# Optimization experiments

Hardware: AMD Instinct MI355X
Metric: run time of the kernel (lower is better)

Reference implementation:

```python
import jax, jax.numpy as jnp
import numpy as np

BN_EPS = 1e-5
N_IN, N_OUT = 200000, 400000
K, M, C_IN, C_OUT = 27, 100000, 64, 64


def setup_inputs() -> dict:
    key = jax.random.key(0)
    ks = jax.random.split(key, 4)
    x = jax.random.normal(ks[0], (N_IN, C_IN), dtype=jnp.float32)
    W = jax.random.normal(ks[1], (K, C_IN, C_OUT), dtype=jnp.float32) * 0.05
    gamma = jnp.ones((C_OUT,), dtype=jnp.float32)
    beta = jnp.zeros((C_OUT,), dtype=jnp.float32)
    in_idx = jax.random.randint(ks[2], (K, M), 0, N_IN, dtype=jnp.int32)
    out_idx = jax.random.randint(ks[3], (K, M), 0, N_OUT, dtype=jnp.int32)
    return {"x": x, "W": W, "gamma": gamma, "beta": beta,
            "in_idx": in_idx, "out_idx": out_idx, "n_out": N_OUT}


def reference(x, W, gamma, beta, in_idx, out_idx, n_out):
    # Sparse transposed conv via gather-GEMM-scatter over K kernel offsets.
    feats = x[in_idx]                               # [K, M, C_in] gather
    contrib = jnp.einsum('kmi,kio->kmo', feats, W)  # per-offset GEMM
    out = jnp.zeros((n_out, contrib.shape[-1]), dtype=x.dtype)
    out = out.at[out_idx.reshape(-1)].add(contrib.reshape(-1, contrib.shape[-1]))
    # BatchNorm (training-mode batch stats over all output points), gamma=1, beta=0 at init.
    mean = jnp.mean(out, axis=0)
    var = jnp.var(out, axis=0)
    y = (out - mean) * jax.lax.rsqrt(var + BN_EPS) * gamma + beta
    return jax.nn.relu(y)
```

## Files before the change

kernel.cpp:

```cpp
#include <hip/hip_runtime.h>
#include <hip/hip_bf16.h>

#define K_OFF 27
#define M_PTS 100000
#define C_CH 64
#define N_OUT_PTS 400000
#define BN_EPS 1e-5f

#define TILE_PTS 16
#define NT (M_PTS / TILE_PTS)
#define BLKX 32
#define WSTRIDE (BLKX * 4)

typedef __attribute__((ext_vector_type(8))) short short8;
typedef __attribute__((ext_vector_type(4))) float f32x4;

__device__ inline void pk_atomic_add_bf16(__hip_bfloat16* p, int bits) {
#if __has_builtin(__builtin_amdgcn_global_atomic_fadd_v2bf16)
    typedef short s2v __attribute__((ext_vector_type(2)));
    typedef __attribute__((address_space(1))) s2v* gp;
    s2v v;
    __builtin_memcpy(&v, &bits, 4);
    __builtin_amdgcn_global_atomic_fadd_v2bf16((gp)(unsigned long long)p, v);
#else
    asm volatile("global_atomic_pk_add_bf16 %0, %1, off"
                 :: "v"((unsigned long long)p), "v"(bits) : "memory");
#endif
}

__device__ inline short bf16c(float f) {
    return __builtin_bit_cast(short, __float2bfloat16(f));
}

__device__ __attribute__((always_inline)) inline void tile_compute(
    const float4* cur, const int* dstv, const short8 bfrag[2][4],
    __hip_bfloat16* __restrict__ out_ws, int c)
{
    short8 af0, af1;
    #pragma unroll
    for (int j = 0; j < 4; ++j) {
        af0[j]     = bf16c(cur[0][j]);
        af0[j + 4] = bf16c(cur[1][j]);
        af1[j]     = bf16c(cur[2][j]);
        af1[j + 4] = bf16c(cur[3][j]);
    }
    f32x4 acc[4];
    #pragma unroll
    for (int tt = 0; tt < 4; ++tt) {
        f32x4 z = {0.f, 0.f, 0.f, 0.f};
        z       = __builtin_amdgcn_mfma_f32_16x16x32_bf16(af0, bfrag[0][tt], z, 0, 0, 0);
        acc[tt] = __builtin_amdgcn_mfma_f32_16x16x32_bf16(af1, bfrag[1][tt], z, 0, 0, 0);
    }
    #pragma unroll
    for (int e = 0; e < 4; ++e) {
        __hip_bfloat16* rp = out_ws + (size_t)dstv[e] * C_CH + 4 * c;
        union { __hip_bfloat162 h; int i; } p0, p1;
        p0.h = __hip_bfloat162(__float2bfloat16(acc[0][e]), __float2bfloat16(acc[1][e]));
        p1.h = __hip_bfloat162(__float2bfloat16(acc[2][e]), __float2bfloat16(acc[3][e]));
        pk_atomic_add_bf16(rp, p0.i);
        pk_atomic_add_bf16(rp + 2, p1.i);
    }
}

__global__ __launch_bounds__(256, 4) void scatter_gemm(
    const float* __restrict__ x, const float* __restrict__ W,
    const int* __restrict__ in_idx, const int* __restrict__ out_idx,
    __hip_bfloat16* __restrict__ out_ws)
{
    const int k = blockIdx.y;
    const int lane = threadIdx.x & 63;
    const int wave = threadIdx.x >> 6;
    const int g = lane >> 4;
    const int c = lane & 15;

    const float* __restrict__ Wk = W + (size_t)k * C_CH * C_CH;
    short8 bfrag[2][4];
    #pragma unroll
    for (int s = 0; s < 2; ++s) {
        #pragma unroll
        for (int tt = 0; tt < 4; ++tt) {
            short8 v;
            #pragma unroll
            for (int j = 0; j < 8; ++j)
                v[j] = bf16c(Wk[(size_t)(32 * s + 8 * g + j) * C_CH + 4 * c + tt]);
            bfrag[s][tt] = v;
        }
    }

    const int kbase = k * M_PTS;
    const int t0 = blockIdx.x * 4 + wave;

    int src_c = in_idx[kbase + t0 * TILE_PTS + c];
    int dstv[4];
    #pragma unroll
    for (int e = 0; e < 4; ++e)
        dstv[e] = out_idx[kbase + t0 * TILE_PTS + 4 * g + e];
    float4 cur[4];
    {
        const float4* xr = (const float4*)x + (size_t)src_c * 16;
        cur[0] = xr[2 * g];     cur[1] = xr[2 * g + 1];
        cur[2] = xr[8 + 2 * g]; cur[3] = xr[8 + 2 * g + 1];
    }
    int src_n = (t0 + WSTRIDE < NT) ? in_idx[kbase + (t0 + WSTRIDE) * TILE_PTS + c] : 0;

    int t = t0;
    for (; t + WSTRIDE < NT; t += WSTRIDE) {
        const int tn = t + WSTRIDE;
        float4 nxt[4]; int dstn[4];
        {
            const float4* xr = (const float4*)x + (size_t)src_n * 16;
            nxt[0] = xr[2 * g];     nxt[1] = xr[2 * g + 1];
            nxt[2] = xr[8 + 2 * g]; nxt[3] = xr[8 + 2 * g + 1];
            #pragma unroll
            for (int e = 0; e < 4; ++e)
                dstn[e] = out_idx[kbase + tn * TILE_PTS + 4 * g + e];
        }
        const int t2 = tn + WSTRIDE;
        const int src_2 = (t2 < NT) ? in_idx[kbase + t2 * TILE_PTS + c] : 0;

        tile_compute(cur, dstv, bfrag, out_ws, c);

        #pragma unroll
        for (int j = 0; j < 4; ++j) cur[j] = nxt[j];
        #pragma unroll
        for (int e = 0; e < 4; ++e) dstv[e] = dstn[e];
        src_c = src_n;
        src_n = src_2;
    }
    tile_compute(cur, dstv, bfrag, out_ws, c);
}

__global__ __launch_bounds__(256) void bn_stats(
    const __hip_bfloat16* __restrict__ ws, float* __restrict__ stats)
{
    const uint4* in = (const uint4*)ws;
    const size_t n = (size_t)N_OUT_PTS * C_CH / 8;
    const size_t stride = (size_t)gridDim.x * blockDim.x;
    float s[8], s2[8];
    #pragma unroll
    for (int j = 0; j < 8; ++j) { s[j] = 0.f; s2[j] = 0.f; }
    for (size_t i = (size_t)blockIdx.x * blockDim.x + threadIdx.x; i < n; i += stride) {
        uint4 q = in[i];
        unsigned wds[4] = {q.x, q.y, q.z, q.w};
        #pragma unroll
        for (int j = 0; j < 4; ++j) {
            __hip_bfloat162 h = *(__hip_bfloat162*)&wds[j];
            float f0 = __low2float(h), f1 = __high2float(h);
            s[2 * j] += f0;  s2[2 * j] += f0 * f0;
            s[2 * j + 1] += f1; s2[2 * j + 1] += f1 * f1;
        }
    }
    __shared__ float sh[2][256][8];
    #pragma unroll
    for (int j = 0; j < 8; ++j) { sh[0][threadIdx.x][j] = s[j]; sh[1][threadIdx.x][j] = s2[j]; }
    __syncthreads();
    if (threadIdx.x < C_CH) {
        const int c = threadIdx.x;
        float ts = 0.f, t2 = 0.f;
        #pragma unroll
        for (int q = 0; q < 32; ++q) {
            ts += sh[0][8 * q + (c >> 3)][c & 7];
            t2 += sh[1][8 * q + (c >> 3)][c & 7];
        }
        unsafeAtomicAdd(&stats[c], ts);
        unsafeAtomicAdd(&stats[C_CH + c], t2);
    }
}

__global__ __launch_bounds__(256) void bn_apply(
    const __hip_bfloat16* __restrict__ ws, const float* __restrict__ stats,
    const float* __restrict__ gamma, const float* __restrict__ beta,
    float* __restrict__ out)
{
    const float inv_n = 1.0f / (float)N_OUT_PTS;
    const int c0 = 8 * (threadIdx.x & 7);
    float sc[8], bs[8];
    #pragma unroll
    for (int j = 0; j < 8; ++j) {
        int c = c0 + j;
        float mean = stats[c] * inv_n;
        float var = stats[C_CH + c] * inv_n - mean * mean;
        float s = gamma[c] * rsqrtf(var + BN_EPS);
        sc[j] = s;
        bs[j] = beta[c] - mean * s;
    }
    const uint4* in = (const uint4*)ws;
    float4* o4 = (float4*)out;
    const size_t n = (size_t)N_OUT_PTS * C_CH / 8;
    const size_t stride = (size_t)gridDim.x * blockDim.x;
    for (size_t i = (size_t)blockIdx.x * blockDim.x + threadIdx.x; i < n; i += stride) {
        uint4 q = in[i];
        unsigned wds[4] = {q.x, q.y, q.z, q.w};
        float f[8];
        #pragma unroll
        for (int j = 0; j < 4; ++j) {
            __hip_bfloat162 h = *(__hip_bfloat162*)&wds[j];
            f[2 * j] = __low2float(h);
            f[2 * j + 1] = __high2float(h);
        }
        float4 r0, r1;
        r0.x = fmaxf(fmaf(f[0], sc[0], bs[0]), 0.f);
        r0.y = fmaxf(fmaf(f[1], sc[1], bs[1]), 0.f);
        r0.z = fmaxf(fmaf(f[2], sc[2], bs[2]), 0.f);
        r0.w = fmaxf(fmaf(f[3], sc[3], bs[3]), 0.f);
        r1.x = fmaxf(fmaf(f[4], sc[4], bs[4]), 0.f);
        r1.y = fmaxf(fmaf(f[5], sc[5], bs[5]), 0.f);
        r1.z = fmaxf(fmaf(f[6], sc[6], bs[6]), 0.f);
        r1.w = fmaxf(fmaf(f[7], sc[7], bs[7]), 0.f);
        o4[2 * i] = r0;
        o4[2 * i + 1] = r1;
    }
}

extern "C" void kernel_launch(void* const* d_in, const int* in_sizes, int n_in,
                              void* d_out, int out_size, void* d_ws, size_t ws_size,
                              hipStream_t stream) {
    const float* x      = (const float*)d_in[0];
    const float* W      = (const float*)d_in[1];
    const float* gamma  = (const float*)d_in[2];
    const float* beta   = (const float*)d_in[3];
    const int*   in_idx = (const int*)d_in[4];
    const int*   out_idx= (const int*)d_in[5];
    float* out = (float*)d_out;

    __hip_bfloat16* out_ws = (__hip_bfloat16*)d_ws;
    const size_t acc_elems = (size_t)N_OUT_PTS * C_CH;
    float* stats = (float*)((char*)d_ws + acc_elems * sizeof(__hip_bfloat16));

    const size_t clear_bytes = acc_elems * sizeof(__hip_bfloat16) + 2 * C_CH * sizeof(float);
    (void)hipMemsetAsync(d_ws, 0, clear_bytes, stream);

    dim3 g1(BLKX, K_OFF);
    scatter_gemm<<<g1, 256, 0, stream>>>(x, W, in_idx, out_idx, out_ws);

    bn_stats<<<2048, 256, 0, stream>>>(out_ws, stats);

    bn_apply<<<2048, 256, 0, stream>>>(out_ws, stats, gamma, beta, out);
}
```

Measured before the change: 766.2 us.

## Replace atomic scatter with binned gather: dense contrib GEMM plus per-output reduction

```diff
diff --git a/kernel.cpp b/kernel.cpp
--- a/kernel.cpp
+++ b/kernel.cpp
@@ -3,17 +3,26 @@
 
 #define K_OFF 27
 #define M_PTS 100000
+#define KM (K_OFF * M_PTS)
 #define C_CH 64
 #define N_OUT_PTS 400000
 #define BN_EPS 1e-5f
 
 #define TILE_PTS 16
 #define NT (M_PTS / TILE_PTS)
-#define BLKX 32
+#define BLKX 64
 #define WSTRIDE (BLKX * 4)
+#define CAP 40
 
 typedef __attribute__((ext_vector_type(8))) short short8;
 typedef __attribute__((ext_vector_type(4))) float f32x4;
+
+__device__ inline short bf16c(float f) {
+    return __builtin_bit_cast(short, __float2bfloat16(f));
+}
+__device__ inline float b2f(unsigned short u) {
+    return __builtin_bit_cast(float, (unsigned)u << 16);
+}
 
 __device__ inline void pk_atomic_add_bf16(__hip_bfloat16* p, int bits) {
 #if __has_builtin(__builtin_amdgcn_global_atomic_fadd_v2bf16)
@@ -28,13 +37,8 @@
 #endif
 }
 
-__device__ inline short bf16c(float f) {
-    return __builtin_bit_cast(short, __float2bfloat16(f));
-}
-
-__device__ __attribute__((always_inline)) inline void tile_compute(
-    const float4* cur, const int* dstv, const short8 bfrag[2][4],
-    __hip_bfloat16* __restrict__ out_ws, int c)
+__device__ __attribute__((always_inline)) inline void tile_mfma(
+    const float4* cur, const short8 bfrag[2][4], f32x4 acc[4])
 {
     short8 af0, af1;
     #pragma unroll
@@ -44,37 +48,17 @@
         af1[j]     = bf16c(cur[2][j]);
         af1[j + 4] = bf16c(cur[3][j]);
     }
-    f32x4 acc[4];
     #pragma unroll
     for (int tt = 0; tt < 4; ++tt) {
         f32x4 z = {0.f, 0.f, 0.f, 0.f};
         z       = __builtin_amdgcn_mfma_f32_16x16x32_bf16(af0, bfrag[0][tt], z, 0, 0, 0);
         acc[tt] = __builtin_amdgcn_mfma_f32_16x16x32_bf16(af1, bfrag[1][tt], z, 0, 0, 0);
     }
-    #pragma unroll
-    for (int e = 0; e < 4; ++e) {
-        __hip_bfloat16* rp = out_ws + (size_t)dstv[e] * C_CH + 4 * c;
-        union { __hip_bfloat162 h; int i; } p0, p1;
-        p0.h = __hip_bfloat162(__float2bfloat16(acc[0][e]), __float2bfloat16(acc[1][e]));
-        p1.h = __hip_bfloat162(__float2bfloat16(acc[2][e]), __float2bfloat16(acc[3][e]));
-        pk_atomic_add_bf16(rp, p0.i);
-        pk_atomic_add_bf16(rp + 2, p1.i);
-    }
-}
-
-__global__ __launch_bounds__(256, 4) void scatter_gemm(
-    const float* __restrict__ x, const float* __restrict__ W,
-    const int* __restrict__ in_idx, const int* __restrict__ out_idx,
-    __hip_bfloat16* __restrict__ out_ws)
-{
-    const int k = blockIdx.y;
-    const int lane = threadIdx.x & 63;
-    const int wave = threadIdx.x >> 6;
-    const int g = lane >> 4;
-    const int c = lane & 15;
-
-    const float* __restrict__ Wk = W + (size_t)k * C_CH * C_CH;
-    short8 bfrag[2][4];
+}
+
+__device__ __attribute__((always_inline)) inline void load_bfrag(
+    const float* __restrict__ Wk, int g, int c, short8 bfrag[2][4])
+{
     #pragma unroll
     for (int s = 0; s < 2; ++s) {
         #pragma unroll
@@ -86,15 +70,37 @@
             bfrag[s][tt] = v;
         }
     }
+}
+
+
+__global__ __launch_bounds__(256) void bin_fill(
+    const int* __restrict__ out_idx, int* __restrict__ counts,
+    int* __restrict__ entries)
+{
+    int i = blockIdx.x * 256 + threadIdx.x;
+    if (i >= KM) return;
+    int o = out_idx[i];
+    int pos = atomicAdd(&counts[o], 1);
+    if (pos < CAP) entries[(size_t)o * CAP + pos] = i;
+}
+
+__global__ __launch_bounds__(256, 4) void contrib_gemm(
+    const float* __restrict__ x, const float* __restrict__ W,
+    const int* __restrict__ in_idx, unsigned short* __restrict__ contrib)
+{
+    const int k = blockIdx.y;
+    const int lane = threadIdx.x & 63;
+    const int wave = threadIdx.x >> 6;
+    const int g = lane >> 4;
+    const int c = lane & 15;
+
+    short8 bfrag[2][4];
+    load_bfrag(W + (size_t)k * C_CH * C_CH, g, c, bfrag);
 
     const int kbase = k * M_PTS;
     const int t0 = blockIdx.x * 4 + wave;
 
     int src_c = in_idx[kbase + t0 * TILE_PTS + c];
-    int dstv[4];
-    #pragma unroll
-    for (int e = 0; e < 4; ++e)
-        dstv[e] = out_idx[kbase + t0 * TILE_PTS + 4 * g + e];
     float4 cur[4];
     {
         const float4* xr = (const float4*)x + (size_t)src_c * 16;
@@ -106,31 +112,169 @@
     int t = t0;
     for (; t + WSTRIDE < NT; t += WSTRIDE) {
         const int tn = t + WSTRIDE;
-        float4 nxt[4]; int dstn[4];
+        float4 nxt[4];
         {
             const float4* xr = (const float4*)x + (size_t)src_n * 16;
             nxt[0] = xr[2 * g];     nxt[1] = xr[2 * g + 1];
             nxt[2] = xr[8 + 2 * g]; nxt[3] = xr[8 + 2 * g + 1];
-            #pragma unroll
-            for (int e = 0; e < 4; ++e)
-                dstn[e] = out_idx[kbase + tn * TILE_PTS + 4 * g + e];
         }
         const int t2 = tn + WSTRIDE;
         const int src_2 = (t2 < NT) ? in_idx[kbase + t2 * TILE_PTS + c] : 0;
 
-        tile_compute(cur, dstv, bfrag, out_ws, c);
+        f32x4 acc[4];
+        tile_mfma(cur, bfrag, acc);
+        const size_t ebase = (size_t)(kbase + t * TILE_PTS);
+        #pragma unroll
+        for (int e = 0; e < 4; ++e) {
+            union { __hip_bfloat162 h; unsigned u; } p0, p1;
+            p0.h = __hip_bfloat162(__float2bfloat16(acc[0][e]), __float2bfloat16(acc[1][e]));
+            p1.h = __hip_bfloat162(__float2bfloat16(acc[2][e]), __float2bfloat16(acc[3][e]));
+            uint2 wv; wv.x = p0.u; wv.y = p1.u;
+            *(uint2*)(contrib + (ebase + 4 * g + e) * C_CH + 4 * c) = wv;
+        }
 
         #pragma unroll
         for (int j = 0; j < 4; ++j) cur[j] = nxt[j];
-        #pragma unroll
-        for (int e = 0; e < 4; ++e) dstv[e] = dstn[e];
-        src_c = src_n;
         src_n = src_2;
     }
-    tile_compute(cur, dstv, bfrag, out_ws, c);
-}
-
-__global__ __launch_bounds__(256) void bn_stats(
+    {
+        f32x4 acc[4];
+        tile_mfma(cur, bfrag, acc);
+        const size_t ebase = (size_t)(kbase + t * TILE_PTS);
+        #pragma unroll
+        for (int e = 0; e < 4; ++e) {
+            union { __hip_bfloat162 h; unsigned u; } p0, p1;
+            p0.h = __hip_bfloat162(__float2bfloat16(acc[0][e]), __float2bfloat16(acc[1][e]));
+            p1.h = __hip_bfloat162(__float2bfloat16(acc[2][e]), __float2bfloat16(acc[3][e]));
+            uint2 wv; wv.x = p0.u; wv.y = p1.u;
+            *(uint2*)(contrib + (ebase + 4 * g + e) * C_CH + 4 * c) = wv;
+        }
+    }
+}
+
+__global__ __launch_bounds__(256) void gather_bn(
+    const unsigned short* __restrict__ contrib, const int* __restrict__ counts,
+    const int* __restrict__ entries, float* __restrict__ preact,
+    float* __restrict__ stats)
+{
+    const int lane = threadIdx.x & 63;
+    const int wave = threadIdx.x >> 6;
+    const int g = lane >> 4;
+    const int c4 = lane & 15;
+
+    float s0 = 0.f, s1 = 0.f, s2 = 0.f, s3 = 0.f;
+    float q0 = 0.f, q1 = 0.f, q2 = 0.f, q3 = 0.f;
+
+    for (int r = blockIdx.x * 16 + wave * 4 + g; r < N_OUT_PTS; r += gridDim.x * 16) {
+        int cnt = counts[r];
+        cnt = cnt > CAP ? CAP : cnt;
+        const int* ep = entries + (size_t)r * CAP;
+        float a0 = 0.f, a1 = 0.f, a2 = 0.f, a3 = 0.f;
+        for (int j = 0; j < cnt; ++j) {
+            int e = ep[j];
+            ushort4 v = *(const ushort4*)(contrib + (size_t)e * C_CH + 4 * c4);
+            a0 += b2f(v.x); a1 += b2f(v.y); a2 += b2f(v.z); a3 += b2f(v.w);
+        }
+        float4 w; w.x = a0; w.y = a1; w.z = a2; w.w = a3;
+        *(float4*)(preact + (size_t)r * C_CH + 4 * c4) = w;
+        s0 += a0; s1 += a1; s2 += a2; s3 += a3;
+        q0 += a0 * a0; q1 += a1 * a1; q2 += a2 * a2; q3 += a3 * a3;
+    }
+
+    __shared__ float sh[2][256][4];
+    sh[0][threadIdx.x][0] = s0; sh[0][threadIdx.x][1] = s1;
+    sh[0][threadIdx.x][2] = s2; sh[0][threadIdx.x][3] = s3;
+    sh[1][threadIdx.x][0] = q0; sh[1][threadIdx.x][1] = q1;
+    sh[1][threadIdx.x][2] = q2; sh[1][threadIdx.x][3] = q3;
+    __syncthreads();
+    if (threadIdx.x < C_CH) {
+        const int ch = threadIdx.x;
+        const int cc = ch >> 2, jj = ch & 3;
+        float ts = 0.f, tq = 0.f;
+        #pragma unroll
+        for (int u = 0; u < 16; ++u) {
+            ts += sh[0][16 * u + cc][jj];
+            tq += sh[1][16 * u + cc][jj];
+        }
+        unsafeAtomicAdd(&stats[ch], ts);
+        unsafeAtomicAdd(&stats[C_CH + ch], tq);
+    }
+}
+
+__global__ __launch_bounds__(256) void bn_apply_f32(
+    float* __restrict__ out, const float* __restrict__ stats,
+    const float* __restrict__ gamma, const float* __restrict__ beta)
+{
+    const float inv_n = 1.0f / (float)N_OUT_PTS;
+    const int c0 = 8 * (threadIdx.x & 7);
+    float sc[8], bs[8];
+    #pragma unroll
+    for (int j = 0; j < 8; ++j) {
+        int ch = c0 + j;
+        float mean = stats[ch] * inv_n;
+        float var = stats[C_CH + ch] * inv_n - mean * mean;
+        float s = gamma[ch] * rsqrtf(var + BN_EPS);
+        sc[j] = s;
+        bs[j] = beta[ch] - mean * s;
+    }
+    float4* o4 = (float4*)out;
+    const size_t n = (size_t)N_OUT_PTS * C_CH / 8;
+    const size_t stride = (size_t)gridDim.x * blockDim.x;
+    for (size_t i = (size_t)blockIdx.x * blockDim.x + threadIdx.x; i < n; i += stride) {
+        float4 r0 = o4[2 * i], r1 = o4[2 * i + 1];
+        r0.x = fmaxf(fmaf(r0.x, sc[0], bs[0]), 0.f);
+        r0.y = fmaxf(fmaf(r0.y, sc[1], bs[1]), 0.f);
+        r0.z = fmaxf(fmaf(r0.z, sc[2], bs[2]), 0.f);
+        r0.w = fmaxf(fmaf(r0.w, sc[3], bs[3]), 0.f);
+        r1.x = fmaxf(fmaf(r1.x, sc[4], bs[4]), 0.f);
+        r1.y = fmaxf(fmaf(r1.y, sc[5], bs[5]), 0.f);
+        r1.z = fmaxf(fmaf(r1.z, sc[6], bs[6]), 0.f);
+        r1.w = fmaxf(fmaf(r1.w, sc[7], bs[7]), 0.f);
+        o4[2 * i] = r0;
+        o4[2 * i + 1] = r1;
+    }
+}
+
+__global__ __launch_bounds__(256, 4) void scatter_gemm_fb(
+    const float* __restrict__ x, const float* __restrict__ W,
+    const int* __restrict__ in_idx, const int* __restrict__ out_idx,
+    __hip_bfloat16* __restrict__ out_ws)
+{
+    const int k = blockIdx.y;
+    const int lane = threadIdx.x & 63;
+    const int wave = threadIdx.x >> 6;
+    const int g = lane >> 4;
+    const int c = lane & 15;
+
+    short8 bfrag[2][4];
+    load_bfrag(W + (size_t)k * C_CH * C_CH, g, c, bfrag);
+
+    const int kbase = k * M_PTS;
+    for (int t = blockIdx.x * 4 + wave; t < NT; t += WSTRIDE) {
+        int src = in_idx[kbase + t * TILE_PTS + c];
+        float4 cur[4];
+        const float4* xr = (const float4*)x + (size_t)src * 16;
+        cur[0] = xr[2 * g];     cur[1] = xr[2 * g + 1];
+        cur[2] = xr[8 + 2 * g]; cur[3] = xr[8 + 2 * g + 1];
+        int dstv[4];
+        #pragma unroll
+        for (int e = 0; e < 4; ++e)
+            dstv[e] = out_idx[kbase + t * TILE_PTS + 4 * g + e];
+        f32x4 acc[4];
+        tile_mfma(cur, bfrag, acc);
+        #pragma unroll
+        for (int e = 0; e < 4; ++e) {
+            __hip_bfloat16* rp = out_ws + (size_t)dstv[e] * C_CH + 4 * c;
+            union { __hip_bfloat162 h; int i; } p0, p1;
+            p0.h = __hip_bfloat162(__float2bfloat16(acc[0][e]), __float2bfloat16(acc[1][e]));
+            p1.h = __hip_bfloat162(__float2bfloat16(acc[2][e]), __float2bfloat16(acc[3][e]));
+            pk_atomic_add_bf16(rp, p0.i);
+            pk_atomic_add_bf16(rp + 2, p1.i);
+        }
+    }
+}
+
+__global__ __launch_bounds__(256) void bn_stats_fb(
     const __hip_bfloat16* __restrict__ ws, float* __restrict__ stats)
 {
     const uint4* in = (const uint4*)ws;
@@ -167,7 +311,7 @@
     }
 }
 
-__global__ __launch_bounds__(256) void bn_apply(
+__global__ __launch_bounds__(256) void bn_apply_fb(
     const __hip_bfloat16* __restrict__ ws, const float* __restrict__ stats,
     const float* __restrict__ gamma, const float* __restrict__ beta,
     float* __restrict__ out)
@@ -223,17 +367,34 @@
     const int*   out_idx= (const int*)d_in[5];
     float* out = (float*)d_out;
 
-    __hip_bfloat16* out_ws = (__hip_bfloat16*)d_ws;
-    const size_t acc_elems = (size_t)N_OUT_PTS * C_CH;
-    float* stats = (float*)((char*)d_ws + acc_elems * sizeof(__hip_bfloat16));
-
-    const size_t clear_bytes = acc_elems * sizeof(__hip_bfloat16) + 2 * C_CH * sizeof(float);
-    (void)hipMemsetAsync(d_ws, 0, clear_bytes, stream);
-
-    dim3 g1(BLKX, K_OFF);
-    scatter_gemm<<<g1, 256, 0, stream>>>(x, W, in_idx, out_idx, out_ws);
-
-    bn_stats<<<2048, 256, 0, stream>>>(out_ws, stats);
-
-    bn_apply<<<2048, 256, 0, stream>>>(out_ws, stats, gamma, beta, out);
-}
+    const size_t CONTRIB_B = (size_t)KM * C_CH * 2;
+    const size_t COUNTS_B  = (size_t)N_OUT_PTS * 4;
+    const size_t ENTRIES_B = (size_t)N_OUT_PTS * CAP * 4;
+    const size_t STATS_B   = 2 * C_CH * sizeof(float);
+    const size_t NEEDED = CONTRIB_B + COUNTS_B + ENTRIES_B + STATS_B;
+
+    if (ws_size >= NEEDED) {
+        unsigned short* contrib = (unsigned short*)d_ws;
+        int* counts = (int*)((char*)d_ws + CONTRIB_B);
+        int* entries = (int*)((char*)d_ws + CONTRIB_B + COUNTS_B);
+        float* stats = (float*)((char*)d_ws + CONTRIB_B + COUNTS_B + ENTRIES_B);
+
+        (void)hipMemsetAsync(counts, 0, COUNTS_B, stream);
+        (void)hipMemsetAsync(stats, 0, STATS_B, stream);
+
+        bin_fill<<<(KM + 255) / 256, 256, 0, stream>>>(out_idx, counts, entries);
+        contrib_gemm<<<dim3(BLKX, K_OFF), 256, 0, stream>>>(x, W, in_idx, contrib);
+        gather_bn<<<12800, 256, 0, stream>>>(contrib, counts, entries, out, stats);
+        bn_apply_f32<<<2048, 256, 0, stream>>>(out, stats, gamma, beta);
+    } else {
+        __hip_bfloat16* out_ws = (__hip_bfloat16*)d_ws;
+        const size_t acc_elems = (size_t)N_OUT_PTS * C_CH;
+        float* stats = (float*)((char*)d_ws + acc_elems * sizeof(__hip_bfloat16));
+        const size_t clear_bytes = acc_elems * sizeof(__hip_bfloat16) + STATS_B;
+        (void)hipMemsetAsync(d_ws, 0, clear_bytes, stream);
+
+        scatter_gemm_fb<<<dim3(BLKX, K_OFF), 256, 0, stream>>>(x, W, in_idx, out_idx, out_ws);
+        bn_stats_fb<<<2048, 256, 0, stream>>>(out_ws, stats);
+        bn_apply_fb<<<2048, 256, 0, stream>>>(out_ws, stats, gamma, beta, out);
+    }
+}
```

After: 768.0 us. No clear change (+0.2%).
